# Kernel tuning notes

Measured on AMD Instinct MI355X. Metric: run time of the kernel, lower is better.

The kernel has to match this reference:

```python
import jax, jax.numpy as jnp
import numpy as np

# Winograd F(2x2, 3x3) transform matrices
_BT = np.array([[1, 0, -1, 0],
                [0, 1,  1, 0],
                [0, -1, 1, 0],
                [0, 1,  0, -1]], dtype=np.float32)
_G = np.array([[1.0, 0.0, 0.0],
               [0.5, 0.5, 0.5],
               [0.5, -0.5, 0.5],
               [0.0, 0.0, 1.0]], dtype=np.float32)
_AT = np.array([[1, 1, 1, 0],
                [0, 1, -1, -1]], dtype=np.float32)


def setup_inputs() -> dict:
    key = jax.random.key(0)
    k1, k2, k3 = jax.random.split(key, 3)
    B, Cin, Cout, H, W = 16, 128, 256, 64, 64
    X = jax.random.normal(k1, (B, Cin, H, W), dtype=jnp.float32)
    # kaiming-uniform-ish scale for a 3x3 conv
    fan_in = Cin * 9
    bound = 1.0 / np.sqrt(fan_in)
    weight = jax.random.uniform(k2, (Cout, Cin, 3, 3), dtype=jnp.float32,
                                minval=-bound * np.sqrt(3.0), maxval=bound * np.sqrt(3.0))
    bias = jax.random.uniform(k3, (Cout,), dtype=jnp.float32, minval=-bound, maxval=bound)
    return {"X": X, "weight": weight, "bias": bias}


def reference(X, weight, bias):
    # Winograd F(2x2,3x3) convolution, stride 1, padding 1 ('same').
    BT = jnp.asarray(_BT, X.dtype)
    G = jnp.asarray(_G, X.dtype)
    AT = jnp.asarray(_AT, X.dtype)
    Bn, C, H, W = X.shape
    K = weight.shape[0]
    tH, tW = H // 2, W // 2  # number of 2x2 output tiles per dim

    xp = jnp.pad(X, ((0, 0), (0, 0), (1, 1), (1, 1)))
    # overlapping 4x4 input tiles with stride 2 -> [B, C, tH, tW, 4, 4]
    rows = (jnp.arange(tH) * 2)[:, None] + jnp.arange(4)[None, :]  # [tH,4]
    cols = (jnp.arange(tW) * 2)[:, None] + jnp.arange(4)[None, :]  # [tW,4]
    d = xp[:, :, rows[:, None, :, None], cols[None, :, None, :]]   # [B,C,tH,tW,4,4]

    # input transform V = B^T d B
    V = jnp.einsum('px,bcijxy,qy->bcijpq', BT, d, BT)
    # filter transform U = G g G^T -> [K,C,4,4]
    U = jnp.einsum('px,kcxy,qy->kcpq', G, weight, G)
    # elementwise product in transform domain, contracted over input channels
    M = jnp.einsum('kcpq,bcijpq->bkijpq', U, V)
    # inverse transform Y = A^T M A -> 2x2 output tiles
    Y = jnp.einsum('px,bkijxy,qy->bkijpq', AT, M, AT)  # [B,K,tH,tW,2,2]

    out = Y.transpose(0, 1, 2, 4, 3, 5).reshape(Bn, K, H, W)
    return out + bias[None, :, None, None]
```

## Files before the change

### kernel.cpp

```cpp
#include <hip/hip_runtime.h>
#include <hip/hip_bf16.h>
#include <cstdint>

#define CIN   128
#define COUT  256
#define BATCH 16
#define HH    64
#define WW    64
#define TH    32
#define TW    32
#define NT    (BATCH*TH*TW)
#define APQ   (COUT*CIN)
#define BPQ   (NT*CIN)

typedef __bf16 bf16x8 __attribute__((ext_vector_type(8)));
typedef float  f32x4  __attribute__((ext_vector_type(4)));

__device__ __forceinline__ void gload16(const void* g, void* l) {
    __builtin_amdgcn_global_load_lds(
        (const __attribute__((address_space(1))) uint32_t*)g,
        (__attribute__((address_space(3))) uint32_t*)l, 16, 0, 0);
}

__global__ __launch_bounds__(256) void wg_wtrans(const float* __restrict__ w,
                                                 __hip_bfloat16* __restrict__ U) {
    int idx = blockIdx.x * 256 + threadIdx.x;
    if (idx >= COUT * CIN) return;
    const float* wp = w + idx * 9;
    float g[3][3];
#pragma unroll
    for (int x = 0; x < 3; x++)
#pragma unroll
        for (int y = 0; y < 3; y++) g[x][y] = wp[x * 3 + y];

    float t[4][3];
#pragma unroll
    for (int y = 0; y < 3; y++) {
        t[0][y] = g[0][y];
        t[1][y] = 0.5f * (g[0][y] + g[1][y] + g[2][y]);
        t[2][y] = 0.5f * (g[0][y] - g[1][y] + g[2][y]);
        t[3][y] = g[2][y];
    }
#pragma unroll
    for (int p = 0; p < 4; p++) {
        float u0 = t[p][0];
        float u1 = 0.5f * (t[p][0] + t[p][1] + t[p][2]);
        float u2 = 0.5f * (t[p][0] - t[p][1] + t[p][2]);
        float u3 = t[p][2];
        U[(p * 4 + 0) * APQ + idx] = __float2bfloat16(u0);
        U[(p * 4 + 1) * APQ + idx] = __float2bfloat16(u1);
        U[(p * 4 + 2) * APQ + idx] = __float2bfloat16(u2);
        U[(p * 4 + 3) * APQ + idx] = __float2bfloat16(u3);
    }
}

__global__ __launch_bounds__(1024) void wg_itrans2(const float* __restrict__ X,
                                                   __hip_bfloat16* __restrict__ V) {
    __shared__ __hip_bfloat16 Xp[128 * 266];
    const int i = blockIdx.x;
    const int b = blockIdx.y;
    const int tid = threadIdx.x;

    {
        int c = tid >> 3, r = (tid >> 1) & 3, e = tid & 1;
        Xp[c * 266 + r * 66 + e * 65] = __float2bfloat16(0.f);
    }
#pragma unroll
    for (int it = 0; it < 8; ++it) {
        int flat = it * 4096 + tid * 4;
        int c = flat >> 8, r = (flat >> 6) & 3, x = flat & 63;
        int y = 2 * i - 1 + r;
        float4 v = make_float4(0.f, 0.f, 0.f, 0.f);
        if (y >= 0 && y < HH)
            v = *reinterpret_cast<const float4*>(&X[(((b * CIN + c) * HH + y) << 6) + x]);
        int base = c * 266 + r * 66 + 1 + x;
        Xp[base + 0] = __float2bfloat16(v.x);
        Xp[base + 1] = __float2bfloat16(v.y);
        Xp[base + 2] = __float2bfloat16(v.z);
        Xp[base + 3] = __float2bfloat16(v.w);
    }
    __syncthreads();

    const int c  = tid & 127;
    const int jj = tid >> 7;
#pragma unroll
    for (int jl = 0; jl < 4; ++jl) {
        const int j = jj * 4 + jl;
        float d[4][4];
#pragma unroll
        for (int r = 0; r < 4; r++) {
            int off = c * 266 + r * 66 + 2 * j;
            ushort2 s01 = *reinterpret_cast<const ushort2*>(&Xp[off]);
            ushort2 s23 = *reinterpret_cast<const ushort2*>(&Xp[off + 2]);
            d[r][0] = __bfloat162float(*reinterpret_cast<__hip_bfloat16*>(&s01.x));
            d[r][1] = __bfloat162float(*reinterpret_cast<__hip_bfloat16*>(&s01.y));
            d[r][2] = __bfloat162float(*reinterpret_cast<__hip_bfloat16*>(&s23.x));
            d[r][3] = __bfloat162float(*reinterpret_cast<__hip_bfloat16*>(&s23.y));
        }
        float t0[4], t1[4], t2[4], t3[4];
#pragma unroll
        for (int y = 0; y < 4; y++) {
            t0[y] = d[0][y] - d[2][y];
            t1[y] = d[1][y] + d[2][y];
            t2[y] = d[2][y] - d[1][y];
            t3[y] = d[1][y] - d[3][y];
        }
        float vm[4][4];
#pragma unroll
        for (int p = 0; p < 4; p++) {
            const float* tp = (p == 0) ? t0 : (p == 1) ? t1 : (p == 2) ? t2 : t3;
            vm[p][0] = tp[0] - tp[2];
            vm[p][1] = tp[1] + tp[2];
            vm[p][2] = tp[2] - tp[1];
            vm[p][3] = tp[1] - tp[3];
        }
        const int bij = (b << 10) + (i << 5) + j;
        const size_t vo = (size_t)bij * CIN + c;
#pragma unroll
        for (int p = 0; p < 4; p++)
#pragma unroll
            for (int q = 0; q < 4; q++)
                V[(size_t)(p * 4 + q) * BPQ + vo] = __float2bfloat16(vm[p][q]);
    }
}

#define ABYTES 16384
#define BUFSZ  32768

__global__ __launch_bounds__(512, 2) void wg_gemm13(const __hip_bfloat16* __restrict__ U,
                                                    const __hip_bfloat16* __restrict__ V,
                                                    const float* __restrict__ bias,
                                                    float* __restrict__ out) {
    __shared__ char lds[4 * BUFSZ];

    int orig = blockIdx.x;
    int wgid = (orig & 7) * 32 + (orig >> 3);
    const int mt = wgid & 1, nt = wgid >> 1;
    const int m0 = mt * 128, n0 = nt * 128;

    const int tid  = threadIdx.x;
    const int lane = tid & 63;
    const int wave = tid >> 6;
    const int wm = wave >> 2, wn = wave & 3;

    const __hip_bfloat16* pa[2];
    const __hip_bfloat16* pb[2];
    int ldsA[2], ldsB[2];
#pragma unroll
    for (int ch = 0; ch < 2; ch++) {
        int c = ch * 512 + tid;
        int R = c >> 3;
        int G = (c & 7) ^ (R & 7);
        pa[ch] = U + (m0 + R) * CIN + G * 8;
        pb[ch] = V + (size_t)(n0 + R) * CIN + G * 8;
        ldsA[ch] = c * 16;
        ldsB[ch] = ABYTES + c * 16;
    }

    const int la = lane & 15, hq = lane >> 4, l7 = lane & 7;
    int aoff[2], boff[2];
#pragma unroll
    for (int kk = 0; kk < 2; kk++) {
        int g = (kk * 4 + hq) ^ l7;
        aoff[kk] = (wm * 64 + la) * 128 + (g << 4);
        boff[kk] = ABYTES + (wn * 32 + la) * 128 + (g << 4);
    }

    f32x4 yac[2][2][4][2];
#pragma unroll
    for (int x = 0; x < 2; x++)
#pragma unroll
        for (int y = 0; y < 2; y++)
#pragma unroll
            for (int mi = 0; mi < 4; mi++)
#pragma unroll
                for (int nj = 0; nj < 2; nj++) yac[x][y][mi][nj] = (f32x4){0.f, 0.f, 0.f, 0.f};
    f32x4 mac[4][2];
    const f32x4 fz = (f32x4){0.f, 0.f, 0.f, 0.f};

    bf16x8 aX[4], bX[2], aY[4], bY[2];
    bf16x8 a1[4], b1[2];

    auto stage = [&](int s) {
        char* sb = lds + (s & 3) * BUFSZ;
        const int pq = s >> 1, kb = (s & 1) * 64;
        gload16(pa[0] + pq * APQ + kb, sb + ldsA[0]);
        gload16(pa[1] + pq * APQ + kb, sb + ldsA[1]);
        gload16(pb[0] + (size_t)pq * BPQ + kb, sb + ldsB[0]);
        gload16(pb[1] + (size_t)pq * BPQ + kb, sb + ldsB[1]);
    };

    auto fold = [&](int pq) {
        const int p = pq >> 2, q = pq & 3;
        const float s1p = (p >= 2) ? -1.f : 1.f;
        const float s1q = (q >= 2) ? -1.f : 1.f;
        if (p != 3 && q != 3) {
#pragma unroll
            for (int mi = 0; mi < 4; mi++)
#pragma unroll
                for (int nj = 0; nj < 2; nj++) yac[0][0][mi][nj] += mac[mi][nj];
        }
        if (p != 3 && q != 0) {
#pragma unroll
            for (int mi = 0; mi < 4; mi++)
#pragma unroll
                for (int nj = 0; nj < 2; nj++) yac[0][1][mi][nj] += s1q * mac[mi][nj];
        }
        if (p != 0 && q != 3) {
#pragma unroll
            for (int mi = 0; mi < 4; mi++)
#pragma unroll
                for (int nj = 0; nj < 2; nj++) yac[1][0][mi][nj] += s1p * mac[mi][nj];
        }
        if (p != 0 && q != 0) {
            const float s11 = s1p * s1q;
#pragma unroll
            for (int mi = 0; mi < 4; mi++)
#pragma unroll
                for (int nj = 0; nj < 2; nj++) yac[1][1][mi][nj] += s11 * mac[mi][nj];
        }
    };

#define SLOT(T, AIN, BIN, AOUT, BOUT, VMC, STG, PRE, INIT, LGK2)              \
    {                                                                          \
        const int t_ = (T);                                                    \
        if (STG) stage(t_ + 3);                                                \
        if ((VMC) == 8)      asm volatile("s_waitcnt vmcnt(8)");               \
        else if ((VMC) == 4) asm volatile("s_waitcnt vmcnt(4)");               \
        else if ((VMC) == 0) asm volatile("s_waitcnt vmcnt(0)");               \
        __builtin_amdgcn_s_barrier();                                          \
        __builtin_amdgcn_sched_barrier(0);                                     \
        {                                                                      \
            const char* rb_ = lds + (t_ & 3) * BUFSZ;                          \
            _Pragma("unroll")                                                  \
            for (int mi = 0; mi < 4; mi++)                                     \
                a1[mi] = *reinterpret_cast<const bf16x8*>(rb_ + aoff[1] + mi * 2048); \
            _Pragma("unroll")                                                  \
            for (int nj = 0; nj < 2; nj++)                                     \
                b1[nj] = *reinterpret_cast<const bf16x8*>(rb_ + boff[1] + nj * 2048); \
        }                                                                      \
        __builtin_amdgcn_sched_barrier(0);                                     \
        asm volatile("s_waitcnt lgkmcnt(6)");                                  \
        __builtin_amdgcn_sched_barrier(0);                                     \
        __builtin_amdgcn_s_setprio(1);                                         \
        _Pragma("unroll")                                                      \
        for (int mi = 0; mi < 4; mi++)                                         \
            _Pragma("unroll")                                                  \
            for (int nj = 0; nj < 2; nj++)                                     \
                mac[mi][nj] = __builtin_amdgcn_mfma_f32_16x16x32_bf16(         \
                    AIN[mi], BIN[nj], (INIT) ? fz : mac[mi][nj], 0, 0, 0);     \
        __builtin_amdgcn_s_setprio(0);                                         \
        if (PRE) {                                                             \
            const char* rb2_ = lds + ((t_ + 1) & 3) * BUFSZ;                   \
            _Pragma("unroll")                                                  \
            for (int mi = 0; mi < 4; mi++)                                     \
                AOUT[mi] = *reinterpret_cast<const bf16x8*>(rb2_ + aoff[0] + mi * 2048); \
            _Pragma("unroll")                                                  \
            for (int nj = 0; nj < 2; nj++)                                     \
                BOUT[nj] = *reinterpret_cast<const bf16x8*>(rb2_ + boff[0] + nj * 2048); \
        }                                                                      \
        __builtin_amdgcn_sched_barrier(0);                                     \
        if ((LGK2) == 6) asm volatile("s_waitcnt lgkmcnt(6)");                 \
        else             asm volatile("s_waitcnt lgkmcnt(0)");                 \
        __builtin_amdgcn_sched_barrier(0);                                     \
        __builtin_amdgcn_s_setprio(1);                                         \
        _Pragma("unroll")                                                      \
        for (int mi = 0; mi < 4; mi++)                                         \
            _Pragma("unroll")                                                  \
            for (int nj = 0; nj < 2; nj++)                                     \
                mac[mi][nj] = __builtin_amdgcn_mfma_f32_16x16x32_bf16(         \
                    a1[mi], b1[nj], mac[mi][nj], 0, 0, 0);                     \
        __builtin_amdgcn_s_setprio(0);                                         \
        __builtin_amdgcn_sched_barrier(0);                                     \
        __builtin_amdgcn_s_barrier();                                          \
    }

    stage(0); stage(1); stage(2);
    asm volatile("s_waitcnt vmcnt(8)");
    __builtin_amdgcn_s_barrier();
    {
        const char* rb_ = lds;
#pragma unroll
        for (int mi = 0; mi < 4; mi++)
            aX[mi] = *reinterpret_cast<const bf16x8*>(rb_ + aoff[0] + mi * 2048);
#pragma unroll
        for (int nj = 0; nj < 2; nj++)
            bX[nj] = *reinterpret_cast<const bf16x8*>(rb_ + boff[0] + nj * 2048);
    }

    for (int tt = 0; tt < 28; tt += 2) {
        if (tt >= 2) fold((tt >> 1) - 1);
        SLOT(tt,     aX, bX, aY, bY, 8, true, true, true,  6)
        SLOT(tt + 1, aY, bY, aX, bX, 8, true, true, false, 6)
    }
    fold(13);
    SLOT(28, aX, bX, aY, bY, 8,  true,  true,  true,  6)
    SLOT(29, aY, bY, aX, bX, 4,  false, true,  false, 6)
    fold(14);
    SLOT(30, aX, bX, aY, bY, 0,  false, true,  true,  6)
    SLOT(31, aY, bY, aX, bX, -1, false, false, false, 0)
    fold(15);

#undef SLOT

    const int lr = lane & 15, rg = lane >> 4;
#pragma unroll
    for (int mi = 0; mi < 4; mi++) {
#pragma unroll
        for (int r = 0; r < 4; r++) {
            const int kout = m0 + wm * 64 + mi * 16 + rg * 4 + r;
            const float bvv = bias[kout];
#pragma unroll
            for (int nj = 0; nj < 2; nj++) {
                const int bij = n0 + wn * 32 + nj * 16 + lr;
                const int bb = bij >> 10, ti = (bij >> 5) & 31, tj = bij & 31;
                float* op = out + (((size_t)bb * COUT + kout) * HH + 2 * ti) * WW + 2 * tj;
                *reinterpret_cast<float2*>(op) =
                    make_float2(yac[0][0][mi][nj][r] + bvv, yac[0][1][mi][nj][r] + bvv);
                *reinterpret_cast<float2*>(op + WW) =
                    make_float2(yac[1][0][mi][nj][r] + bvv, yac[1][1][mi][nj][r] + bvv);
            }
        }
    }
}

extern "C" void kernel_launch(void* const* d_in, const int* in_sizes, int n_in,
                              void* d_out, int out_size, void* d_ws, size_t ws_size,
                              hipStream_t stream) {
    const float* X    = (const float*)d_in[0];
    const float* w    = (const float*)d_in[1];
    const float* bias = (const float*)d_in[2];
    float* out        = (float*)d_out;

    __hip_bfloat16* U = (__hip_bfloat16*)d_ws;
    __hip_bfloat16* V = (__hip_bfloat16*)((char*)d_ws + (1u << 20));

    wg_wtrans<<<(COUT * CIN + 255) / 256, 256, 0, stream>>>(w, U);
    wg_itrans2<<<dim3(TH, BATCH), 1024, 0, stream>>>(X, V);
    wg_gemm13<<<(COUT / 128) * (NT / 128), 512, 0, stream>>>(U, V, bias, out);
}
```

Measured before the change: 67.44 us.

## Merge filter transform into input-transform launch and simplify GEMM k-loop schedule

```diff
diff --git a/kernel.cpp b/kernel.cpp
--- a/kernel.cpp
+++ b/kernel.cpp
@@ -22,10 +22,9 @@
         (__attribute__((address_space(3))) uint32_t*)l, 16, 0, 0);
 }
 
-__global__ __launch_bounds__(256) void wg_wtrans(const float* __restrict__ w,
-                                                 __hip_bfloat16* __restrict__ U) {
-    int idx = blockIdx.x * 256 + threadIdx.x;
-    if (idx >= COUT * CIN) return;
+__device__ __forceinline__ void wtrans_one(const float* __restrict__ w,
+                                           __hip_bfloat16* __restrict__ U,
+                                           int idx) {
     const float* wp = w + idx * 9;
     float g[3][3];
 #pragma unroll
@@ -54,12 +53,20 @@
     }
 }
 
-__global__ __launch_bounds__(1024) void wg_itrans2(const float* __restrict__ X,
-                                                   __hip_bfloat16* __restrict__ V) {
-    __shared__ __hip_bfloat16 Xp[128 * 266];
+__global__ __launch_bounds__(1024) void wg_itrans3(const float* __restrict__ X,
+                                                   const float* __restrict__ w,
+                                                   __hip_bfloat16* __restrict__ V,
+                                                   __hip_bfloat16* __restrict__ U) {
     const int i = blockIdx.x;
     const int b = blockIdx.y;
     const int tid = threadIdx.x;
+
+    if (b == BATCH) {
+        wtrans_one(w, U, i * 1024 + tid);
+        return;
+    }
+
+    __shared__ __hip_bfloat16 Xp[128 * 266];
 
     {
         int c = tid >> 3, r = (tid >> 1) & 3, e = tid & 1;
@@ -127,7 +134,7 @@
 #define ABYTES 16384
 #define BUFSZ  32768
 
-__global__ __launch_bounds__(512, 2) void wg_gemm13(const __hip_bfloat16* __restrict__ U,
+__global__ __launch_bounds__(512, 2) void wg_gemm17(const __hip_bfloat16* __restrict__ U,
                                                     const __hip_bfloat16* __restrict__ V,
                                                     const float* __restrict__ bias,
                                                     float* __restrict__ out) {
@@ -178,9 +185,6 @@
     f32x4 mac[4][2];
     const f32x4 fz = (f32x4){0.f, 0.f, 0.f, 0.f};
 
-    bf16x8 aX[4], bX[2], aY[4], bY[2];
-    bf16x8 a1[4], b1[2];
-
     auto stage = [&](int s) {
         char* sb = lds + (s & 3) * BUFSZ;
         const int pq = s >> 1, kb = (s & 1) * 64;
@@ -221,87 +225,48 @@
         }
     };
 
-#define SLOT(T, AIN, BIN, AOUT, BOUT, VMC, STG, PRE, INIT, LGK2)              \
-    {                                                                          \
-        const int t_ = (T);                                                    \
-        if (STG) stage(t_ + 3);                                                \
-        if ((VMC) == 8)      asm volatile("s_waitcnt vmcnt(8)");               \
-        else if ((VMC) == 4) asm volatile("s_waitcnt vmcnt(4)");               \
-        else if ((VMC) == 0) asm volatile("s_waitcnt vmcnt(0)");               \
-        __builtin_amdgcn_s_barrier();                                          \
-        __builtin_amdgcn_sched_barrier(0);                                     \
-        {                                                                      \
-            const char* rb_ = lds + (t_ & 3) * BUFSZ;                          \
-            _Pragma("unroll")                                                  \
-            for (int mi = 0; mi < 4; mi++)                                     \
-                a1[mi] = *reinterpret_cast<const bf16x8*>(rb_ + aoff[1] + mi * 2048); \
-            _Pragma("unroll")                                                  \
-            for (int nj = 0; nj < 2; nj++)                                     \
-                b1[nj] = *reinterpret_cast<const bf16x8*>(rb_ + boff[1] + nj * 2048); \
-        }                                                                      \
-        __builtin_amdgcn_sched_barrier(0);                                     \
-        asm volatile("s_waitcnt lgkmcnt(6)");                                  \
-        __builtin_amdgcn_sched_barrier(0);                                     \
-        __builtin_amdgcn_s_setprio(1);                                         \
-        _Pragma("unroll")                                                      \
-        for (int mi = 0; mi < 4; mi++)                                         \
-            _Pragma("unroll")                                                  \
-            for (int nj = 0; nj < 2; nj++)                                     \
-                mac[mi][nj] = __builtin_amdgcn_mfma_f32_16x16x32_bf16(         \
-                    AIN[mi], BIN[nj], (INIT) ? fz : mac[mi][nj], 0, 0, 0);     \
-        __builtin_amdgcn_s_setprio(0);                                         \
-        if (PRE) {                                                             \
-            const char* rb2_ = lds + ((t_ + 1) & 3) * BUFSZ;                   \
-            _Pragma("unroll")                                                  \
-            for (int mi = 0; mi < 4; mi++)                                     \
-                AOUT[mi] = *reinterpret_cast<const bf16x8*>(rb2_ + aoff[0] + mi * 2048); \
-            _Pragma("unroll")                                                  \
-            for (int nj = 0; nj < 2; nj++)                                     \
-                BOUT[nj] = *reinterpret_cast<const bf16x8*>(rb2_ + boff[0] + nj * 2048); \
-        }                                                                      \
-        __builtin_amdgcn_sched_barrier(0);                                     \
-        if ((LGK2) == 6) asm volatile("s_waitcnt lgkmcnt(6)");                 \
-        else             asm volatile("s_waitcnt lgkmcnt(0)");                 \
-        __builtin_amdgcn_sched_barrier(0);                                     \
-        __builtin_amdgcn_s_setprio(1);                                         \
-        _Pragma("unroll")                                                      \
-        for (int mi = 0; mi < 4; mi++)                                         \
-            _Pragma("unroll")                                                  \
-            for (int nj = 0; nj < 2; nj++)                                     \
-                mac[mi][nj] = __builtin_amdgcn_mfma_f32_16x16x32_bf16(         \
-                    a1[mi], b1[nj], mac[mi][nj], 0, 0, 0);                     \
-        __builtin_amdgcn_s_setprio(0);                                         \
-        __builtin_amdgcn_sched_barrier(0);                                     \
-        __builtin_amdgcn_s_barrier();                                          \
-    }
-
     stage(0); stage(1); stage(2);
-    asm volatile("s_waitcnt vmcnt(8)");
-    __builtin_amdgcn_s_barrier();
-    {
-        const char* rb_ = lds;
+
+#pragma unroll
+    for (int t = 0; t < 32; ++t) {
+        if (t <= 28) stage(t + 3);
+
+        if (t <= 28)      asm volatile("s_waitcnt vmcnt(8)" ::: "memory");
+        else if (t == 29) asm volatile("s_waitcnt vmcnt(4)" ::: "memory");
+        else if (t == 30) asm volatile("s_waitcnt vmcnt(0)" ::: "memory");
+        __builtin_amdgcn_s_barrier();
+
+        const char* rb = lds + (t & 3) * BUFSZ;
+        bf16x8 a0[4], b0[2], a1[4], b1[2];
+#pragma unroll
+        for (int mi = 0; mi < 4; mi++) {
+            a0[mi] = *reinterpret_cast<const bf16x8*>(rb + aoff[0] + mi * 2048);
+            a1[mi] = *reinterpret_cast<const bf16x8*>(rb + aoff[1] + mi * 2048);
+        }
+#pragma unroll
+        for (int nj = 0; nj < 2; nj++) {
+            b0[nj] = *reinterpret_cast<const bf16x8*>(rb + boff[0] + nj * 2048);
+            b1[nj] = *reinterpret_cast<const bf16x8*>(rb + boff[1] + nj * 2048);
+        }
+
+        const bool init = (t & 1) == 0;
 #pragma unroll
         for (int mi = 0; mi < 4; mi++)
-            aX[mi] = *reinterpret_cast<const bf16x8*>(rb_ + aoff[0] + mi * 2048);
-#pragma unroll
-        for (int nj = 0; nj < 2; nj++)
-            bX[nj] = *reinterpret_cast<const bf16x8*>(rb_ + boff[0] + nj * 2048);
-    }
-
-    for (int tt = 0; tt < 28; tt += 2) {
-        if (tt >= 2) fold((tt >> 1) - 1);
-        SLOT(tt,     aX, bX, aY, bY, 8, true, true, true,  6)
-        SLOT(tt + 1, aY, bY, aX, bX, 8, true, true, false, 6)
-    }
-    fold(13);
-    SLOT(28, aX, bX, aY, bY, 8,  true,  true,  true,  6)
-    SLOT(29, aY, bY, aX, bX, 4,  false, true,  false, 6)
-    fold(14);
-    SLOT(30, aX, bX, aY, bY, 0,  false, true,  true,  6)
-    SLOT(31, aY, bY, aX, bX, -1, false, false, false, 0)
-    fold(15);
-
-#undef SLOT
+#pragma unroll
+            for (int nj = 0; nj < 2; nj++)
+                mac[mi][nj] = __builtin_amdgcn_mfma_f32_16x16x32_bf16(
+                    a0[mi], b0[nj], init ? fz : mac[mi][nj], 0, 0, 0);
+#pragma unroll
+        for (int mi = 0; mi < 4; mi++)
+#pragma unroll
+            for (int nj = 0; nj < 2; nj++)
+                mac[mi][nj] = __builtin_amdgcn_mfma_f32_16x16x32_bf16(
+                    a1[mi], b1[nj], mac[mi][nj], 0, 0, 0);
+
+        if (t & 1) fold(t >> 1);
+
+        __builtin_amdgcn_s_barrier();
+    }
 
     const int lr = lane & 15, rg = lane >> 4;
 #pragma unroll
@@ -335,7 +300,6 @@
     __hip_bfloat16* U = (__hip_bfloat16*)d_ws;
     __hip_bfloat16* V = (__hip_bfloat16*)((char*)d_ws + (1u << 20));
 
-    wg_wtrans<<<(COUT * CIN + 255) / 256, 256, 0, stream>>>(w, U);
-    wg_itrans2<<<dim3(TH, BATCH), 1024, 0, stream>>>(X, V);
-    wg_gemm13<<<(COUT / 128) * (NT / 128), 512, 0, stream>>>(U, V, bias, out);
-}
+    wg_itrans3<<<dim3(TH, BATCH + 1), 1024, 0, stream>>>(X, w, V, U);
+    wg_gemm17<<<(COUT / 128) * (NT / 128), 512, 0, stream>>>(U, V, bias, out);
+}
```

Result: slower. 196.0 us (+190.7%).
